# Kernel optimization log

Measured on AMD Instinct MI355X. Metric: run time of the kernel, lower is better.

## Reference

```python
import jax, jax.numpy as jnp
import numpy as np

B, T, N, DIN, D = 8, 20, 1000, 64, 64


def setup_inputs() -> dict:
    key = jax.random.key(0)
    ks = jax.random.split(key, 10)
    stdv = 1.0 / np.sqrt(DIN + D)  # torch reset_param: uniform(-1/sqrt(in_size), ...)
    def gate_w(k):
        return jax.random.uniform(k, (N, DIN + D, D), jnp.float32, -stdv, stdv)
    x = jax.random.normal(ks[0], (B, T, N, DIN), jnp.float32)
    # xavier_normal_ for time_att.W [N, T, D]: fan_in=T*D, fan_out=N*D
    xav_std = np.sqrt(2.0 / (T * D + N * D)).astype(np.float32)
    Wt = jax.random.normal(ks[5], (N, T, D), jnp.float32) * xav_std
    return {
        "x": x,
        "Wi": gate_w(ks[1]), "bi": jnp.zeros((N, D), jnp.float32),
        "Wo": gate_w(ks[2]), "bo": jnp.zeros((N, D), jnp.float32),
        "Wf": gate_w(ks[3]), "bf": jnp.zeros((N, D), jnp.float32),
        "Wc": gate_w(ks[4]), "bc": jnp.zeros((N, D), jnp.float32),
        "Wt": Wt,
    }


def _lstm_att(x, Wi, bi, Wo, bo, Wf, bf, Wc, bc, Wt):
    b, t, n, din = x.shape
    d = Wi.shape[-1]

    def gate(xh, W, bias):
        # per-stock matmul: [b,n,din+d] x [n,din+d,d] -> [b,n,d]
        return jnp.einsum('bni,nio->bno', xh, W) + bias

    def step(carry, xt):
        h, c = carry  # [b,n,d]
        xh = jnp.concatenate([xt, h], axis=-1)
        it = jax.nn.sigmoid(gate(xh, Wi, bi))
        ot = jax.nn.sigmoid(gate(xh, Wo, bo))
        ft = jax.nn.sigmoid(gate(xh, Wf, bf))
        ch = jnp.tanh(gate(xh, Wc, bc))
        c2 = ft * c + it * ch
        h2 = ot * jnp.tanh(c2)
        return (h2, c2), h2

    h0 = jnp.zeros((b, n, d), x.dtype)
    c0 = jnp.zeros((b, n, d), x.dtype)
    xt_seq = jnp.swapaxes(x, 0, 1)  # [t,b,n,din]
    _, hs = jax.lax.scan(step, (h0, c0), xt_seq)
    h = jnp.swapaxes(hs, 0, 1)  # [b,t,n,d] (torch.stack dim=-3)

    # time attention
    h_bntd = jnp.swapaxes(h, 1, 2)  # [b,n,t,d]
    scores = jnp.sum(h_bntd * Wt, axis=-1)  # [b,n,t]
    att = jax.nn.softmax(scores, axis=-1)
    out = jnp.einsum('bnt,bntd->bnd', att, h_bntd)  # matmul([b,n,1,t],[b,n,t,d]).squeeze()
    return out  # [b,n,d]


def reference(x, Wi, bi, Wo, bo, Wf, bf, Wc, bc, Wt):
    return _lstm_att(x, Wi, bi, Wo, bo, Wf, bf, Wc, bc, Wt)
```

## Files before the change

kernel.cpp:

```cpp
#include <hip/hip_runtime.h>

#define TT 20
#define NSTK 1000
#define THREADS 256

typedef float f32x4 __attribute__((ext_vector_type(4)));
typedef _Float16 f16x8 __attribute__((ext_vector_type(8)));
typedef _Float16 f16x2 __attribute__((ext_vector_type(2)));

__device__ __forceinline__ float rcp_f(float x) { return __builtin_amdgcn_rcpf(x); }
__device__ __forceinline__ float sigmoid_f(float x) { return rcp_f(1.0f + __expf(-x)); }
__device__ __forceinline__ float tanh_f(float x) {
    return 1.0f - 2.0f * rcp_f(__expf(2.0f * x) + 1.0f);
}

#define AIDX(kf, q, row, j) ((((kf) * 4 + (q)) * 16 + (row)) * 8 + (j))

extern "C" __global__ void __launch_bounds__(THREADS, 3)
lstm_att_f16(const float* __restrict__ x,
             const float* __restrict__ Wi, const float* __restrict__ bi,
             const float* __restrict__ Wo, const float* __restrict__ bo,
             const float* __restrict__ Wf, const float* __restrict__ bf_,
             const float* __restrict__ Wc, const float* __restrict__ bc,
             const float* __restrict__ Wt,
             float* __restrict__ out)
{
    __shared__ __align__(16) _Float16 afrag[2048];
    __shared__ __align__(16) _Float16 hhist[TT * 8 * 64];
    __shared__ __align__(16) float    wtlds[TT * 64];

    const int n    = blockIdx.x;
    const int tid  = threadIdx.x;
    const int lane = tid & 63;
    const int w    = tid >> 6;
    const int q    = lane >> 4;
    const int r16  = lane & 15;
    const int dcol = w * 16 + r16;
    const int g4   = q * 4;

    f16x8 bw[4][4];
    {
        const float* Wg[4] = {Wi, Wo, Wf, Wc};
        #pragma unroll
        for (int g = 0; g < 4; ++g) {
            const float* base = Wg[g] + (size_t)n * 8192 + dcol;
            #pragma unroll
            for (int kf = 0; kf < 4; ++kf)
                #pragma unroll
                for (int j = 0; j < 8; ++j)
                    bw[g][kf][j] = (_Float16)base[(kf * 32 + q * 8 + j) * 64];
        }
    }
    float biasv[4];
    biasv[0] = bi[n * 64 + dcol];
    biasv[1] = bo[n * 64 + dcol];
    biasv[2] = bf_[n * 64 + dcol];
    biasv[3] = bc[n * 64 + dcol];

    #pragma unroll
    for (int u = 0; u < 5; ++u)
        wtlds[tid + u * THREADS] = Wt[(size_t)n * (TT * 64) + tid + u * THREADS];
    #pragma unroll
    for (int u = 0; u < 4; ++u)
        afrag[1024 + tid + u * THREADS] = (_Float16)0.0f;

    const int sb = tid >> 5, dx = (tid & 31) * 2;
    const int skf = dx >> 5, skk = dx & 31;
    const int sbase = AIDX(skf, skk >> 3, sb, skk & 7);
    const float* xptr = x + ((size_t)sb * TT * NSTK + (size_t)n) * 64 + dx;
    float2 xreg = *(const float2*)xptr;

    float cst[4] = {0.f, 0.f, 0.f, 0.f};
    float hv[4];

    __syncthreads();

    for (int t = 0; t < TT; ++t) {
        *(f16x2*)(afrag + sbase) = (f16x2){(_Float16)xreg.x, (_Float16)xreg.y};
        const int tn = (t + 1 < TT) ? t + 1 : t;
        xreg = *(const float2*)(xptr + (size_t)tn * NSTK * 64);
        __syncthreads();

        f16x8 af[4];
        #pragma unroll
        for (int kf = 0; kf < 4; ++kf)
            af[kf] = *(const f16x8*)(afrag + AIDX(kf, q, r16, 0));

        f32x4 acc[4];
        #pragma unroll
        for (int g = 0; g < 4; ++g)
            acc[g] = (f32x4){biasv[g], biasv[g], biasv[g], biasv[g]};
        #pragma unroll
        for (int kf = 0; kf < 4; ++kf) {
            #pragma unroll
            for (int g = 0; g < 4; ++g)
                acc[g] = __builtin_amdgcn_mfma_f32_16x16x32_f16(af[kf], bw[g][kf], acc[g], 0, 0, 0);
        }

        if (lane < 32) {
            #pragma unroll
            for (int r = 0; r < 4; ++r) {
                const float ig = sigmoid_f(acc[0][r]);
                const float og = sigmoid_f(acc[1][r]);
                const float fg = sigmoid_f(acc[2][r]);
                const float cg = tanh_f(acc[3][r]);
                const float cn = fmaf(fg, cst[r], ig * cg);
                cst[r] = cn;
                hv[r] = og * tanh_f(cn);
                hhist[(t * 8 + g4 + r) * 64 + dcol] = (_Float16)hv[r];
            }
        }
        __syncthreads();

        if (lane < 32) {
            const int kfh = 2 + (dcol >> 5), kkh = dcol & 31;
            const int hb = AIDX(kfh, kkh >> 3, 0, kkh & 7);
            #pragma unroll
            for (int r = 0; r < 4; ++r)
                afrag[hb + (g4 + r) * 8] = (_Float16)hv[r];
        }
    }

    __syncthreads();

    #pragma unroll
    for (int bb = 0; bb < 2; ++bb) {
        const int b = 2 * w + bb;
        float s[TT];
        #pragma unroll
        for (int t = 0; t < TT; ++t)
            s[t] = (float)hhist[(t * 8 + b) * 64 + lane] * wtlds[t * 64 + lane];
        #pragma unroll
        for (int t = 0; t < TT; ++t) {
            #pragma unroll
            for (int mk = 32; mk >= 1; mk >>= 1)
                s[t] += __shfl_xor(s[t], mk, 64);
        }
        float m = s[0];
        #pragma unroll
        for (int t = 1; t < TT; ++t) m = fmaxf(m, s[t]);
        float se = 0.f;
        #pragma unroll
        for (int t = 0; t < TT; ++t) { s[t] = __expf(s[t] - m); se += s[t]; }
        const float rs = rcp_f(se);
        float o = 0.f;
        #pragma unroll
        for (int t = 0; t < TT; ++t)
            o = fmaf(s[t], (float)hhist[(t * 8 + b) * 64 + lane], o);
        out[((size_t)b * NSTK + n) * 64 + lane] = o * rs;
    }
}

extern "C" void kernel_launch(void* const* d_in, const int* in_sizes, int n_in,
                              void* d_out, int out_size, void* d_ws, size_t ws_size,
                              hipStream_t stream) {
    const float* x  = (const float*)d_in[0];
    const float* Wi = (const float*)d_in[1];
    const float* bi = (const float*)d_in[2];
    const float* Wo = (const float*)d_in[3];
    const float* bo = (const float*)d_in[4];
    const float* Wf = (const float*)d_in[5];
    const float* bf = (const float*)d_in[6];
    const float* Wc = (const float*)d_in[7];
    const float* bc = (const float*)d_in[8];
    const float* Wt = (const float*)d_in[9];
    float* out = (float*)d_out;

    lstm_att_f16<<<NSTK, THREADS, 0, stream>>>(
        x, Wi, bi, Wo, bo, Wf, bf, Wc, bc, Wt, out);
}
```

Baseline: 63.46 us.

## Double-buffer A fragment to use one barrier per step and split gate work

```diff
diff --git a/kernel.cpp b/kernel.cpp
--- a/kernel.cpp
+++ b/kernel.cpp
@@ -16,7 +16,7 @@
 
 #define AIDX(kf, q, row, j) ((((kf) * 4 + (q)) * 16 + (row)) * 8 + (j))
 
-extern "C" __global__ void __launch_bounds__(THREADS, 3)
+extern "C" __global__ void __launch_bounds__(THREADS, 4)
 lstm_att_f16(const float* __restrict__ x,
              const float* __restrict__ Wi, const float* __restrict__ bi,
              const float* __restrict__ Wo, const float* __restrict__ bo,
@@ -25,9 +25,8 @@
              const float* __restrict__ Wt,
              float* __restrict__ out)
 {
-    __shared__ __align__(16) _Float16 afrag[2048];
+    __shared__ __align__(16) _Float16 afrag[2][2048];
     __shared__ __align__(16) _Float16 hhist[TT * 8 * 64];
-    __shared__ __align__(16) float    wtlds[TT * 64];
 
     const int n    = blockIdx.x;
     const int tid  = threadIdx.x;
@@ -36,7 +35,8 @@
     const int q    = lane >> 4;
     const int r16  = lane & 15;
     const int dcol = w * 16 + r16;
-    const int g4   = q * 4;
+    const bool hi  = lane >= 32;
+    const int rowbase = ((lane & 31) >> 4) * 4 + (hi ? 2 : 0);
 
     f16x8 bw[4][4];
     {
@@ -57,34 +57,40 @@
     biasv[2] = bf_[n * 64 + dcol];
     biasv[3] = bc[n * 64 + dcol];
 
-    #pragma unroll
-    for (int u = 0; u < 5; ++u)
-        wtlds[tid + u * THREADS] = Wt[(size_t)n * (TT * 64) + tid + u * THREADS];
-    #pragma unroll
-    for (int u = 0; u < 4; ++u)
-        afrag[1024 + tid + u * THREADS] = (_Float16)0.0f;
+    const int sb = tid >> 5, dx = (tid & 31) * 2;
+    const int sbase = AIDX(dx >> 5, (dx & 31) >> 3, sb, dx & 7);
+    const float* xptr = x + ((size_t)sb * TT * NSTK + (size_t)n) * 64 + dx;
 
-    const int sb = tid >> 5, dx = (tid & 31) * 2;
-    const int skf = dx >> 5, skk = dx & 31;
-    const int sbase = AIDX(skf, skk >> 3, sb, skk & 7);
-    const float* xptr = x + ((size_t)sb * TT * NSTK + (size_t)n) * 64 + dx;
-    float2 xreg = *(const float2*)xptr;
+    {
+        const float2 x0 = *(const float2*)xptr;
+        *(f16x2*)(&afrag[0][sbase]) = (f16x2){(_Float16)x0.x, (_Float16)x0.y};
+        #pragma unroll
+        for (int u = 0; u < 4; ++u)
+            afrag[0][1024 + tid + u * THREADS] = (_Float16)0.0f;
+    }
+    float2 xreg = *(const float2*)(xptr + (size_t)NSTK * 64);
 
-    float cst[4] = {0.f, 0.f, 0.f, 0.f};
-    float hv[4];
+    float cst0 = 0.f, cst1 = 0.f;
 
     __syncthreads();
 
+    const int kfh = 2 + (dcol >> 5), kkh = dcol & 31;
+    const int hb0 = AIDX(kfh, kkh >> 3, rowbase, kkh & 7);
+
     for (int t = 0; t < TT; ++t) {
-        *(f16x2*)(afrag + sbase) = (f16x2){(_Float16)xreg.x, (_Float16)xreg.y};
-        const int tn = (t + 1 < TT) ? t + 1 : t;
-        xreg = *(const float2*)(xptr + (size_t)tn * NSTK * 64);
-        __syncthreads();
+        const int cur = t & 1, nxt = cur ^ 1;
 
         f16x8 af[4];
         #pragma unroll
         for (int kf = 0; kf < 4; ++kf)
-            af[kf] = *(const f16x8*)(afrag + AIDX(kf, q, r16, 0));
+            af[kf] = *(const f16x8*)(&afrag[cur][AIDX(kf, q, r16, 0)]);
+
+        if (t + 1 < TT)
+            *(f16x2*)(&afrag[nxt][sbase]) = (f16x2){(_Float16)xreg.x, (_Float16)xreg.y};
+        {
+            const int tn = (t + 2 < TT) ? t + 2 : TT - 1;
+            xreg = *(const float2*)(xptr + (size_t)tn * NSTK * 64);
+        }
 
         f32x4 acc[4];
         #pragma unroll
@@ -97,39 +103,40 @@
                 acc[g] = __builtin_amdgcn_mfma_f32_16x16x32_f16(af[kf], bw[g][kf], acc[g], 0, 0, 0);
         }
 
-        if (lane < 32) {
-            #pragma unroll
-            for (int r = 0; r < 4; ++r) {
-                const float ig = sigmoid_f(acc[0][r]);
-                const float og = sigmoid_f(acc[1][r]);
-                const float fg = sigmoid_f(acc[2][r]);
-                const float cg = tanh_f(acc[3][r]);
-                const float cn = fmaf(fg, cst[r], ig * cg);
-                cst[r] = cn;
-                hv[r] = og * tanh_f(cn);
-                hhist[(t * 8 + g4 + r) * 64 + dcol] = (_Float16)hv[r];
-            }
+        float p0[4], p1[4];
+        #pragma unroll
+        for (int g = 0; g < 4; ++g) {
+            const float t2 = __shfl_xor(acc[g][2], 32, 64);
+            const float t3 = __shfl_xor(acc[g][3], 32, 64);
+            p0[g] = hi ? t2 : acc[g][0];
+            p1[g] = hi ? t3 : acc[g][1];
         }
+
+        const float ig0 = sigmoid_f(p0[0]), og0 = sigmoid_f(p0[1]);
+        const float fg0 = sigmoid_f(p0[2]), cg0 = tanh_f(p0[3]);
+        const float ig1 = sigmoid_f(p1[0]), og1 = sigmoid_f(p1[1]);
+        const float fg1 = sigmoid_f(p1[2]), cg1 = tanh_f(p1[3]);
+        cst0 = fmaf(fg0, cst0, ig0 * cg0);
+        cst1 = fmaf(fg1, cst1, ig1 * cg1);
+        const float h0 = og0 * tanh_f(cst0);
+        const float h1 = og1 * tanh_f(cst1);
+
+        afrag[nxt][hb0]     = (_Float16)h0;
+        afrag[nxt][hb0 + 8] = (_Float16)h1;
+        hhist[(t * 8 + rowbase) * 64 + dcol]     = (_Float16)h0;
+        hhist[(t * 8 + rowbase + 1) * 64 + dcol] = (_Float16)h1;
+
         __syncthreads();
-
-        if (lane < 32) {
-            const int kfh = 2 + (dcol >> 5), kkh = dcol & 31;
-            const int hb = AIDX(kfh, kkh >> 3, 0, kkh & 7);
-            #pragma unroll
-            for (int r = 0; r < 4; ++r)
-                afrag[hb + (g4 + r) * 8] = (_Float16)hv[r];
-        }
     }
 
-    __syncthreads();
-
+    const float* wtg = Wt + (size_t)n * (TT * 64);
     #pragma unroll
     for (int bb = 0; bb < 2; ++bb) {
         const int b = 2 * w + bb;
         float s[TT];
         #pragma unroll
         for (int t = 0; t < TT; ++t)
-            s[t] = (float)hhist[(t * 8 + b) * 64 + lane] * wtlds[t * 64 + lane];
+            s[t] = (float)hhist[(t * 8 + b) * 64 + lane] * wtg[t * 64 + lane];
         #pragma unroll
         for (int t = 0; t < TT; ++t) {
             #pragma unroll
```

Result: faster. 56.91 us (-10.3%).

## Run each stock's LSTM in a single wavefront with all weights in registers

Applied to the files above, without the earlier changes.

```diff
diff --git a/kernel.cpp b/kernel.cpp
--- a/kernel.cpp
+++ b/kernel.cpp
@@ -2,134 +2,161 @@
 
 #define TT 20
 #define NSTK 1000
-#define THREADS 256
+#define SC_SIG  1.44269504089f
+#define SC_TANH 2.88539008178f
+#define HPAD 72
 
 typedef float f32x4 __attribute__((ext_vector_type(4)));
 typedef _Float16 f16x8 __attribute__((ext_vector_type(8)));
-typedef _Float16 f16x2 __attribute__((ext_vector_type(2)));
 
 __device__ __forceinline__ float rcp_f(float x) { return __builtin_amdgcn_rcpf(x); }
-__device__ __forceinline__ float sigmoid_f(float x) { return rcp_f(1.0f + __expf(-x)); }
-__device__ __forceinline__ float tanh_f(float x) {
-    return 1.0f - 2.0f * rcp_f(__expf(2.0f * x) + 1.0f);
-}
+__device__ __forceinline__ float exp2_f(float x) { return __builtin_amdgcn_exp2f(x); }
 
-#define AIDX(kf, q, row, j) ((((kf) * 4 + (q)) * 16 + (row)) * 8 + (j))
 
-extern "C" __global__ void __launch_bounds__(THREADS, 3)
-lstm_att_f16(const float* __restrict__ x,
-             const float* __restrict__ Wi, const float* __restrict__ bi,
-             const float* __restrict__ Wo, const float* __restrict__ bo,
-             const float* __restrict__ Wf, const float* __restrict__ bf_,
-             const float* __restrict__ Wc, const float* __restrict__ bc,
-             const float* __restrict__ Wt,
-             float* __restrict__ out)
+extern "C" __global__ void __launch_bounds__(64, 1)
+lstm_1wave(const float* __restrict__ x,
+           const float* __restrict__ Wi, const float* __restrict__ bi,
+           const float* __restrict__ Wo, const float* __restrict__ bo,
+           const float* __restrict__ Wf, const float* __restrict__ bf_,
+           const float* __restrict__ Wc, const float* __restrict__ bc,
+           const float* __restrict__ Wt,
+           float* __restrict__ out)
 {
-    __shared__ __align__(16) _Float16 afrag[2048];
-    __shared__ __align__(16) _Float16 hhist[TT * 8 * 64];
-    __shared__ __align__(16) float    wtlds[TT * 64];
+    __shared__ __align__(16) _Float16 hh[TT + 1][8][HPAD];
 
-    const int n    = blockIdx.x;
-    const int tid  = threadIdx.x;
-    const int lane = tid & 63;
-    const int w    = tid >> 6;
+    const int lane = threadIdx.x;
     const int q    = lane >> 4;
     const int r16  = lane & 15;
-    const int dcol = w * 16 + r16;
-    const int g4   = q * 4;
+    const int bsrc = r16 & 7;
+    const bool hi  = lane >= 32;
+    const int rb   = ((lane & 31) >> 4) * 4 + (hi ? 2 : 0);
+    const int n    = blockIdx.x;
 
-    f16x8 bw[4][4];
-    {
-        const float* Wg[4] = {Wi, Wo, Wf, Wc};
+    for (int i = lane; i < 288; i += 64) ((unsigned*)hh)[i] = 0u;
+
+    const float* Wg[4] = {Wi, Wo, Wf, Wc};
+    const float* Bg[4] = {bi, bo, bf_, bc};
+
+    float biasv[4][4];
+    #pragma unroll
+    for (int g = 0; g < 4; ++g) {
+        const float sc = (g == 3) ? SC_TANH : SC_SIG;
         #pragma unroll
-        for (int g = 0; g < 4; ++g) {
-            const float* base = Wg[g] + (size_t)n * 8192 + dcol;
+        for (int cg = 0; cg < 4; ++cg)
+            biasv[g][cg] = Bg[g][n * 64 + cg * 16 + r16] * sc;
+    }
+
+    f16x8 bw[4][4][4];
+    #pragma unroll
+    for (int g = 0; g < 4; ++g) {
+        const float* base = Wg[g] + (size_t)n * 8192 + r16;
+        const float sc = (g == 3) ? SC_TANH : SC_SIG;
+        float tmp[4][4][8];
+        #pragma unroll
+        for (int kf = 0; kf < 4; ++kf)
             #pragma unroll
-            for (int kf = 0; kf < 4; ++kf)
+            for (int cg = 0; cg < 4; ++cg)
                 #pragma unroll
                 for (int j = 0; j < 8; ++j)
-                    bw[g][kf][j] = (_Float16)base[(kf * 32 + q * 8 + j) * 64];
-        }
+                    tmp[kf][cg][j] = base[(kf * 32 + q * 8 + j) * 64 + cg * 16];
+        #pragma unroll
+        for (int kf = 0; kf < 4; ++kf)
+            #pragma unroll
+            for (int cg = 0; cg < 4; ++cg)
+                #pragma unroll
+                for (int j = 0; j < 8; ++j)
+                    bw[g][kf][cg][j] = (_Float16)(tmp[kf][cg][j] * sc);
     }
-    float biasv[4];
-    biasv[0] = bi[n * 64 + dcol];
-    biasv[1] = bo[n * 64 + dcol];
-    biasv[2] = bf_[n * 64 + dcol];
-    biasv[3] = bc[n * 64 + dcol];
 
-    #pragma unroll
-    for (int u = 0; u < 5; ++u)
-        wtlds[tid + u * THREADS] = Wt[(size_t)n * (TT * 64) + tid + u * THREADS];
-    #pragma unroll
-    for (int u = 0; u < 4; ++u)
-        afrag[1024 + tid + u * THREADS] = (_Float16)0.0f;
+    const float* xq = x + ((size_t)(bsrc * TT) * NSTK + n) * 64 + q * 8;
+    float4 xp0 = *(const float4*)(xq);
+    float4 xp1 = *(const float4*)(xq + 4);
+    float4 xp2 = *(const float4*)(xq + 32);
+    float4 xp3 = *(const float4*)(xq + 36);
 
-    const int sb = tid >> 5, dx = (tid & 31) * 2;
-    const int skf = dx >> 5, skk = dx & 31;
-    const int sbase = AIDX(skf, skk >> 3, sb, skk & 7);
-    const float* xptr = x + ((size_t)sb * TT * NSTK + (size_t)n) * 64 + dx;
-    float2 xreg = *(const float2*)xptr;
-
-    float cst[4] = {0.f, 0.f, 0.f, 0.f};
-    float hv[4];
-
-    __syncthreads();
+    float cst0[4] = {0.f, 0.f, 0.f, 0.f};
+    float cst1[4] = {0.f, 0.f, 0.f, 0.f};
 
     for (int t = 0; t < TT; ++t) {
-        *(f16x2*)(afrag + sbase) = (f16x2){(_Float16)xreg.x, (_Float16)xreg.y};
-        const int tn = (t + 1 < TT) ? t + 1 : t;
-        xreg = *(const float2*)(xptr + (size_t)tn * NSTK * 64);
         __syncthreads();
 
         f16x8 af[4];
+        af[2] = *(const f16x8*)&hh[t][bsrc][q * 8];
+        af[3] = *(const f16x8*)&hh[t][bsrc][32 + q * 8];
+        #pragma unroll
+        for (int j = 0; j < 4; ++j) {
+            af[0][j]     = (_Float16)(&xp0.x)[j];
+            af[0][4 + j] = (_Float16)(&xp1.x)[j];
+            af[1][j]     = (_Float16)(&xp2.x)[j];
+            af[1][4 + j] = (_Float16)(&xp3.x)[j];
+        }
+
+        {
+            const size_t off = (size_t)((t + 1 < TT) ? t + 1 : t) * (NSTK * 64);
+            xp0 = *(const float4*)(xq + off);
+            xp1 = *(const float4*)(xq + off + 4);
+            xp2 = *(const float4*)(xq + off + 32);
+            xp3 = *(const float4*)(xq + off + 36);
+        }
+
+        f32x4 acc[4][4];
+        #pragma unroll
+        for (int g = 0; g < 4; ++g)
+            #pragma unroll
+            for (int cg = 0; cg < 4; ++cg)
+                acc[g][cg] = (f32x4){biasv[g][cg], biasv[g][cg], biasv[g][cg], biasv[g][cg]};
+
         #pragma unroll
         for (int kf = 0; kf < 4; ++kf)
-            af[kf] = *(const f16x8*)(afrag + AIDX(kf, q, r16, 0));
+            #pragma unroll
+            for (int g = 0; g < 4; ++g)
+                #pragma unroll
+                for (int cg = 0; cg < 4; ++cg)
+                    acc[g][cg] = __builtin_amdgcn_mfma_f32_16x16x32_f16(
+                        af[kf], bw[g][kf][cg], acc[g][cg], 0, 0, 0);
 
-        f32x4 acc[4];
+        float p0[4][4], p1[4][4];
         #pragma unroll
         for (int g = 0; g < 4; ++g)
-            acc[g] = (f32x4){biasv[g], biasv[g], biasv[g], biasv[g]};
+            #pragma unroll
+            for (int cg = 0; cg < 4; ++cg) {
+                const float u2 = __shfl_xor(acc[g][cg][2], 32, 64);
+                const float u3 = __shfl_xor(acc[g][cg][3], 32, 64);
+                p0[g][cg] = hi ? u2 : acc[g][cg][0];
+                p1[g][cg] = hi ? u3 : acc[g][cg][1];
+            }
+
         #pragma unroll
-        for (int kf = 0; kf < 4; ++kf) {
-            #pragma unroll
-            for (int g = 0; g < 4; ++g)
-                acc[g] = __builtin_amdgcn_mfma_f32_16x16x32_f16(af[kf], bw[g][kf], acc[g], 0, 0, 0);
-        }
-
-        if (lane < 32) {
-            #pragma unroll
-            for (int r = 0; r < 4; ++r) {
-                const float ig = sigmoid_f(acc[0][r]);
-                const float og = sigmoid_f(acc[1][r]);
-                const float fg = sigmoid_f(acc[2][r]);
-                const float cg = tanh_f(acc[3][r]);
-                const float cn = fmaf(fg, cst[r], ig * cg);
-                cst[r] = cn;
-                hv[r] = og * tanh_f(cn);
-                hhist[(t * 8 + g4 + r) * 64 + dcol] = (_Float16)hv[r];
-            }
-        }
-        __syncthreads();
-
-        if (lane < 32) {
-            const int kfh = 2 + (dcol >> 5), kkh = dcol & 31;
-            const int hb = AIDX(kfh, kkh >> 3, 0, kkh & 7);
-            #pragma unroll
-            for (int r = 0; r < 4; ++r)
-                afrag[hb + (g4 + r) * 8] = (_Float16)hv[r];
+        for (int cg = 0; cg < 4; ++cg) {
+            const float ig0 = rcp_f(1.0f + exp2_f(-p0[0][cg]));
+            const float og0 = rcp_f(1.0f + exp2_f(-p0[1][cg]));
+            const float fg0 = rcp_f(1.0f + exp2_f(-p0[2][cg]));
+            const float cg0 = 1.0f - 2.0f * rcp_f(exp2_f(p0[3][cg]) + 1.0f);
+            const float ig1 = rcp_f(1.0f + exp2_f(-p1[0][cg]));
+            const float og1 = rcp_f(1.0f + exp2_f(-p1[1][cg]));
+            const float fg1 = rcp_f(1.0f + exp2_f(-p1[2][cg]));
+            const float cg1 = 1.0f - 2.0f * rcp_f(exp2_f(p1[3][cg]) + 1.0f);
+            cst0[cg] = fmaf(fg0, cst0[cg], ig0 * cg0);
+            cst1[cg] = fmaf(fg1, cst1[cg], ig1 * cg1);
+            const float h0 = og0 * (1.0f - 2.0f * rcp_f(exp2_f(cst0[cg] * SC_TANH) + 1.0f));
+            const float h1 = og1 * (1.0f - 2.0f * rcp_f(exp2_f(cst1[cg] * SC_TANH) + 1.0f));
+            hh[t + 1][rb][cg * 16 + r16]     = (_Float16)h0;
+            hh[t + 1][rb + 1][cg * 16 + r16] = (_Float16)h1;
         }
     }
 
     __syncthreads();
 
+    const float* wtg = Wt + (size_t)n * (TT * 64) + lane;
+    float wtv[TT];
     #pragma unroll
-    for (int bb = 0; bb < 2; ++bb) {
-        const int b = 2 * w + bb;
+    for (int t = 0; t < TT; ++t) wtv[t] = wtg[t * 64];
+
+    for (int b = 0; b < 8; ++b) {
         float s[TT];
         #pragma unroll
         for (int t = 0; t < TT; ++t)
-            s[t] = (float)hhist[(t * 8 + b) * 64 + lane] * wtlds[t * 64 + lane];
+            s[t] = (float)hh[t + 1][b][lane] * wtv[t];
         #pragma unroll
         for (int t = 0; t < TT; ++t) {
             #pragma unroll
@@ -141,12 +168,12 @@
         for (int t = 1; t < TT; ++t) m = fmaxf(m, s[t]);
         float se = 0.f;
         #pragma unroll
-        for (int t = 0; t < TT; ++t) { s[t] = __expf(s[t] - m); se += s[t]; }
+        for (int t = 0; t < TT; ++t) { s[t] = exp2_f((s[t] - m) * SC_SIG); se += s[t]; }
         const float rs = rcp_f(se);
         float o = 0.f;
         #pragma unroll
         for (int t = 0; t < TT; ++t)
-            o = fmaf(s[t], (float)hhist[(t * 8 + b) * 64 + lane], o);
+            o = fmaf(s[t], (float)hh[t + 1][b][lane], o);
         out[((size_t)b * NSTK + n) * 64 + lane] = o * rs;
     }
 }
@@ -166,6 +193,6 @@
     const float* Wt = (const float*)d_in[9];
     float* out = (float*)d_out;
 
-    lstm_att_f16<<<NSTK, THREADS, 0, stream>>>(
+    lstm_1wave<<<NSTK, 64, 0, stream>>>(
         x, Wi, bi, Wo, bo, Wf, bf, Wc, bc, Wt, out);
 }
```

Result: slower. 85.10 us (+34.1%).
